# Performance work log

Hardware: AMD Instinct MI355X
Metric: run time of the kernel (lower is better)

The kernel has to match this reference:

```python
import jax, jax.numpy as jnp
import numpy as np

NUM_USERS = 100000
NUM_ITEMS = 50000
EMBED_DIM = 64
N_LAYERS = 3
NNZ = 4800000
BATCH = 16384
N_NODES = NUM_USERS + NUM_ITEMS


def setup_inputs() -> dict:
    key = jax.random.key(0)
    k1, k2, k3, k4, k5, k6, k7 = jax.random.split(key, 7)
    users = jax.random.randint(k1, (BATCH,), 0, NUM_USERS, dtype=jnp.int64 if jax.config.jax_enable_x64 else jnp.int32)
    items = jax.random.randint(k2, (BATCH,), 0, NUM_ITEMS, dtype=jnp.int64 if jax.config.jax_enable_x64 else jnp.int32)
    adj_rows = jax.random.randint(k3, (NNZ,), 0, N_NODES, dtype=jnp.int32)
    adj_cols = jax.random.randint(k4, (NNZ,), 0, N_NODES, dtype=jnp.int32)
    adj_vals = jax.random.uniform(k5, (NNZ,), dtype=jnp.float32)
    user_emb = jax.random.normal(k6, (NUM_USERS, EMBED_DIM), dtype=jnp.float32)
    item_emb = jax.random.normal(k7, (NUM_ITEMS, EMBED_DIM), dtype=jnp.float32)
    return {"users": users, "items": items, "adj_rows": adj_rows,
            "adj_cols": adj_cols, "adj_vals": adj_vals,
            "user_emb": user_emb, "item_emb": item_emb}


def _spmm(rows, cols, vals, x):
    # y = A @ x for COO sparse A: gather source rows, scale, scatter-add to dest
    return jax.ops.segment_sum(vals[:, None] * x[cols], rows, num_segments=N_NODES)


def reference(users, items, adj_rows, adj_cols, adj_vals, user_emb, item_emb):
    ego = jnp.concatenate([user_emb, item_emb], axis=0)  # [N_NODES, D]
    acc = ego
    cur = ego
    for _ in range(N_LAYERS):
        cur = _spmm(adj_rows, adj_cols, adj_vals, cur)
        acc = acc + cur
    mean_emb = acc / jnp.float32(N_LAYERS + 1)
    user_final = mean_emb[:NUM_USERS]
    item_final = mean_emb[NUM_USERS:]
    u = user_final[users]  # [B, D]
    i = item_final[items]  # [B, D]
    return jnp.sum(u * i, axis=-1)  # [B]
```

## Files before the change

### kernel.cpp

```cpp
#include <hip/hip_runtime.h>
#include <hip/hip_bf16.h>

#define NUM_USERS 100000
#define NUM_ITEMS 50000
#define EMBED_DIM 64
#define N_NODES   150000
#define ROW_SHIFT 9
#define ROWS_PER_BUCKET 512
#define B_BUCKETS ((N_NODES + ROWS_PER_BUCKET - 1) / ROWS_PER_BUCKET)
#define NBP 512
#define BIN_CHUNK 2048
#define COL_MASK 0x3FFFF

typedef unsigned short ushort_t;
typedef unsigned int uint_t;

__device__ __forceinline__ float bf16_to_f32(ushort_t u) {
    return __uint_as_float(((unsigned)u) << 16);
}
__device__ __forceinline__ ushort_t f32_to_bf16(float f) {
    return __builtin_bit_cast(ushort_t, __float2bfloat16(f));
}

__global__ void __launch_bounds__(512) k_bin2(const float* __restrict__ ue,
                                              const float* __restrict__ ie,
                                              ushort_t* __restrict__ xb,
                                              const int* __restrict__ rows,
                                              const int* __restrict__ cols,
                                              const float* __restrict__ vals,
                                              int* __restrict__ cursor,
                                              int2* __restrict__ staging,
                                              int nnz, int cap, int g_conv) {
    int t = threadIdx.x;
    if ((int)blockIdx.x < g_conv) {
        int i = blockIdx.x * 512 + t;
        const int n4 = (N_NODES * EMBED_DIM) / 4;
        if (i >= n4) return;
        const int usplit = (NUM_USERS * EMBED_DIM) / 4;
        float4 f = (i < usplit) ? ((const float4*)ue)[i] : ((const float4*)ie)[i - usplit];
        ushort4 o;
        o.x = f32_to_bf16(f.x);
        o.y = f32_to_bf16(f.y);
        o.z = f32_to_bf16(f.z);
        o.w = f32_to_bf16(f.w);
        ((ushort4*)xb)[i] = o;
        return;
    }

    __shared__ int  ccnt[NBP];
    __shared__ int  cpos[NBP];
    __shared__ int  gdst[NBP];
    __shared__ int2 entries[BIN_CHUNK];
    __shared__ ushort_t ebuck[BIN_CHUNK];

    int base = (blockIdx.x - g_conv) * BIN_CHUNK;
    ccnt[t] = 0;
    __syncthreads();

    int myrow[BIN_CHUNK / 512];
#pragma unroll
    for (int k = 0; k < BIN_CHUNK / 512; k++) {
        int idx = base + k * 512 + t;
        int r = (idx < nnz) ? rows[idx] : -1;
        myrow[k] = r;
        if (r >= 0) atomicAdd(&ccnt[r >> ROW_SHIFT], 1);
    }
    __syncthreads();

    int c = ccnt[t];
    cpos[t] = c;
    __syncthreads();
    for (int d = 1; d < NBP; d <<= 1) {
        int y = (t >= d) ? cpos[t - d] : 0;
        __syncthreads();
        cpos[t] += y;
        __syncthreads();
    }
    int total = cpos[NBP - 1];
    int excl = cpos[t] - c;
    __syncthreads();
    cpos[t] = excl;
    __syncthreads();

#pragma unroll
    for (int k = 0; k < BIN_CHUNK / 512; k++) {
        int r = myrow[k];
        if (r >= 0) {
            int idx = base + k * 512 + t;
            int b = r >> ROW_SHIFT;
            int lrow = r & (ROWS_PER_BUCKET - 1);
            int slot = atomicAdd(&cpos[b], 1);
            entries[slot] = make_int2(cols[idx] | (lrow << 18), __float_as_int(vals[idx]));
            ebuck[slot] = (ushort_t)b;
        }
    }
    __syncthreads();

    if (t < B_BUCKETS && ccnt[t] > 0) {
        int g = atomicAdd(&cursor[t], ccnt[t]);
        gdst[t] = t * cap + g - (cpos[t] - ccnt[t]);
    }
    __syncthreads();

    for (int i = t; i < total; i += 512) {
        int eb = ebuck[i];
        int pos = gdst[eb] + i;
        if (pos < (eb + 1) * cap)
            staging[pos] = entries[i];
    }
}

__global__ void __launch_bounds__(512) k_scatter2b(const int2* __restrict__ staging,
                                                   const int* __restrict__ cursor,
                                                   int2* __restrict__ ranges,
                                                   int2* __restrict__ cv, int cap) {
    __shared__ int rc[ROWS_PER_BUCKET];
    int b = blockIdx.x;
    int t = threadIdx.x;
    int rbase = b * cap;
    int cnt_b = cursor[b];
    if (cnt_b > cap) cnt_b = cap;
    int row0 = b << ROW_SHIFT;

    rc[t] = 0;
    __syncthreads();
    for (int i = t; i < cnt_b; i += 512)
        atomicAdd(&rc[staging[rbase + i].x >> 18], 1);
    __syncthreads();

    int c = rc[t];
    for (int d = 1; d < ROWS_PER_BUCKET; d <<= 1) {
        int y = (t >= d) ? rc[t - d] : 0;
        __syncthreads();
        rc[t] += y;
        __syncthreads();
    }
    int excl = rc[t] - c;
    int row = row0 + t;
    if (row < N_NODES) ranges[row] = make_int2(rbase + excl, rbase + excl + c);
    __syncthreads();
    rc[t] = excl;
    __syncthreads();

    for (int i = t; i < cnt_b; i += 512) {
        int2 e = staging[rbase + i];
        int pos = rbase + atomicAdd(&rc[e.x >> 18], 1);
        cv[pos] = make_int2(e.x & COL_MASK, e.y);
    }
}

#define ISSUE8(R, J0)                                                         \
    _Pragma("unroll")                                                         \
    for (int j = 0; j < 8; j++) {                                             \
        int sc = __builtin_amdgcn_readlane(vc, (J0) + j);                     \
        R[j] = xb[((size_t)(uint_t)sc << 6) + lane];                          \
    }

#define CONS8(R, J0)                                                          \
    _Pragma("unroll")                                                         \
    for (int j = 0; j < 8; j++) {                                             \
        float sv = __uint_as_float((uint_t)__builtin_amdgcn_readlane(vv, (J0) + j)); \
        acc += sv * __uint_as_float((uint_t)R[j] << 16);                      \
    }

__device__ __forceinline__ float spmm_row_rl(int beg, int end, int lane,
                                             const int2* __restrict__ cv,
                                             const ushort_t* __restrict__ xb) {
    float acc = 0.f;
#pragma unroll 1
    for (int b = beg; b < end; b += 64) {
        int2 ed = cv[b + lane];
        bool lv = (b + lane) < end;
        int vc = lv ? ed.x : 0;
        int vv = lv ? ed.y : 0;
        int rem = end - b;
        if (rem > 64) rem = 64;

        ushort_t q0[8], q1[8], q2[8], q3[8];
        ISSUE8(q0, 0)
        if (rem > 8)  { ISSUE8(q1, 8)  }
        if (rem > 16) { ISSUE8(q2, 16) }
        if (rem > 24) { ISSUE8(q3, 24) }
        CONS8(q0, 0)
        if (rem > 8)  { CONS8(q1, 8)  }
        if (rem > 16) { CONS8(q2, 16) }
        if (rem > 24) { CONS8(q3, 24) }
        if (rem > 32) {
            ISSUE8(q0, 32)
            if (rem > 40) { ISSUE8(q1, 40) }
            if (rem > 48) { ISSUE8(q2, 48) }
            if (rem > 56) { ISSUE8(q3, 56) }
            CONS8(q0, 32)
            if (rem > 40) { CONS8(q1, 40) }
            if (rem > 48) { CONS8(q2, 48) }
            if (rem > 56) { CONS8(q3, 56) }
        }
    }
    return acc;
}

__global__ void k_spmm(const int2* __restrict__ ranges, const int2* __restrict__ cv,
                       const ushort_t* __restrict__ xb, ushort_t* __restrict__ out) {
    int row = (blockIdx.x * blockDim.x + threadIdx.x) >> 6;
    int lane = threadIdx.x & 63;
    if (row >= N_NODES) return;
    row = __builtin_amdgcn_readfirstlane(row);
    int2 rng = ranges[row];
    int beg = __builtin_amdgcn_readfirstlane(rng.x);
    int end = __builtin_amdgcn_readfirstlane(rng.y);
    float a = spmm_row_rl(beg, end, lane, cv, xb);
    out[(size_t)row * 64 + lane] = f32_to_bf16(a);
}

__global__ void k_last(const int2* __restrict__ ranges, const int2* __restrict__ cv,
                       const int* __restrict__ users, const int* __restrict__ items,
                       const float* __restrict__ ue, const float* __restrict__ ie,
                       const ushort_t* __restrict__ xbA, const ushort_t* __restrict__ xbB,
                       float* __restrict__ out, int batch) {
    int w = (blockIdx.x * blockDim.x + threadIdx.x) >> 6;
    int lane = threadIdx.x & 63;
    if (w >= batch) return;

    int uu = __builtin_amdgcn_readfirstlane(users[w]);
    int ii = __builtin_amdgcn_readfirstlane(items[w]);
    int row_u = uu;
    int row_i = NUM_USERS + ii;

    int2 ru = ranges[row_u];
    float a_u = spmm_row_rl(__builtin_amdgcn_readfirstlane(ru.x),
                            __builtin_amdgcn_readfirstlane(ru.y), lane, cv, xbB);
    int2 ri = ranges[row_i];
    float a_i = spmm_row_rl(__builtin_amdgcn_readfirstlane(ri.x),
                            __builtin_amdgcn_readfirstlane(ri.y), lane, cv, xbB);

    float e_u = ue[(size_t)uu * EMBED_DIM + lane];
    float e_i = ie[(size_t)ii * EMBED_DIM + lane];
    float Au = bf16_to_f32(xbA[(size_t)row_u * 64 + lane]);
    float Bu = bf16_to_f32(xbB[(size_t)row_u * 64 + lane]);
    float Ai = bf16_to_f32(xbA[(size_t)row_i * 64 + lane]);
    float Bi = bf16_to_f32(xbB[(size_t)row_i * 64 + lane]);

    float ux = e_u + Au + Bu + a_u;
    float ix = e_i + Ai + Bi + a_i;

    float p = ux * ix;
#pragma unroll
    for (int d = 32; d > 0; d >>= 1) p += __shfl_down(p, d, 64);
    if (lane == 0) out[w] = p * (1.0f / 16.0f);
}


extern "C" void kernel_launch(void* const* d_in, const int* in_sizes, int n_in,
                              void* d_out, int out_size, void* d_ws, size_t ws_size,
                              hipStream_t stream) {
    const int*   users    = (const int*)  d_in[0];
    const int*   items    = (const int*)  d_in[1];
    const int*   adj_rows = (const int*)  d_in[2];
    const int*   adj_cols = (const int*)  d_in[3];
    const float* adj_vals = (const float*)d_in[4];
    const float* user_emb = (const float*)d_in[5];
    const float* item_emb = (const float*)d_in[6];
    float* out = (float*)d_out;

    const int batch = in_sizes[0];
    const int nnz   = in_sizes[2];

    int cap = ((nnz / B_BUCKETS) * 9 + 7) / 8;
    cap = (cap + 63) & ~63;
    const size_t padded = (size_t)B_BUCKETS * cap;

    char* p = (char*)d_ws;
    auto alloc = [&](size_t bytes) -> char* {
        char* r = p;
        p += (bytes + 255) & ~(size_t)255;
        return r;
    };
    const size_t xb_bytes = (size_t)N_NODES * EMBED_DIM * 2;
    int2*     ranges = (int2*) alloc((size_t)N_NODES * 8);
    int*      cursor = (int*)  alloc(NBP * 4);
    int2*     cv     = (int2*) alloc(padded * 8);
    size_t    region_bytes = padded * 8;
    if (region_bytes < 2 * xb_bytes) region_bytes = 2 * xb_bytes;
    char*     region  = alloc(region_bytes);
    int2*     staging = (int2*)region;
    ushort_t* xbA     = (ushort_t*)region;
    ushort_t* xbB     = (ushort_t*)(region + xb_bytes);
    ushort_t* xb_ego  = (ushort_t*)alloc(xb_bytes);

    const int g_conv  = ((N_NODES * EMBED_DIM / 4) + 511) / 512;
    const int g_bin   = (nnz + BIN_CHUNK - 1) / BIN_CHUNK;
    const int g_nodes = (N_NODES + 3) / 4;
    const int g_batch = (batch + 3) / 4;

    hipMemsetAsync(cursor, 0, NBP * 4, stream);
    k_bin2<<<g_conv + g_bin, 512, 0, stream>>>(user_emb, item_emb, xb_ego,
                                               adj_rows, adj_cols, adj_vals,
                                               cursor, staging, nnz, cap, g_conv);
    k_scatter2b<<<B_BUCKETS, 512, 0, stream>>>(staging, cursor, ranges, cv, cap);

    k_spmm<<<g_nodes, 256, 0, stream>>>(ranges, cv, xb_ego, xbA);

    k_spmm<<<g_nodes, 256, 0, stream>>>(ranges, cv, xbA, xbB);

    k_last<<<g_batch, 256, 0, stream>>>(ranges, cv, users, items,
                                        user_emb, item_emb, xbA, xbB, out, batch);
}
```

Baseline: 430.1 us.

## Replace bucket binning with per-row count, scan, and atomic placement for CSR build

Replaces the two-stage bucket sort (LDS binning into padded staging, then a per-bucket counting sort) with three passes: global per-row atomic counting, a per-bucket scan that writes row ranges and cursors, and a placement pass that reserves each edge's slot with a global atomic and writes column and value directly. This drops the staging buffer and its extra read and write traffic. In exchange it uses millions of global atomics on 150k counters, twice, and adds a kernel launch plus a larger memset. Edge order within a row becomes nondeterministic, so float summation order can vary between runs.

```diff
diff --git a/kernel.cpp b/kernel.cpp
--- a/kernel.cpp
+++ b/kernel.cpp
@@ -8,9 +8,6 @@
 #define ROW_SHIFT 9
 #define ROWS_PER_BUCKET 512
 #define B_BUCKETS ((N_NODES + ROWS_PER_BUCKET - 1) / ROWS_PER_BUCKET)
-#define NBP 512
-#define BIN_CHUNK 2048
-#define COL_MASK 0x3FFFF
 
 typedef unsigned short ushort_t;
 typedef unsigned int uint_t;
@@ -22,15 +19,12 @@
     return __builtin_bit_cast(ushort_t, __float2bfloat16(f));
 }
 
-__global__ void __launch_bounds__(512) k_bin2(const float* __restrict__ ue,
-                                              const float* __restrict__ ie,
-                                              ushort_t* __restrict__ xb,
-                                              const int* __restrict__ rows,
-                                              const int* __restrict__ cols,
-                                              const float* __restrict__ vals,
-                                              int* __restrict__ cursor,
-                                              int2* __restrict__ staging,
-                                              int nnz, int cap, int g_conv) {
+__global__ void __launch_bounds__(512) k_cc(const float* __restrict__ ue,
+                                            const float* __restrict__ ie,
+                                            ushort_t* __restrict__ xb,
+                                            const int* __restrict__ rows,
+                                            int* __restrict__ rc,
+                                            int nnz, int g_conv) {
     int t = threadIdx.x;
     if ((int)blockIdx.x < g_conv) {
         int i = blockIdx.x * 512 + t;
@@ -46,106 +40,68 @@
         ((ushort4*)xb)[i] = o;
         return;
     }
-
-    __shared__ int  ccnt[NBP];
-    __shared__ int  cpos[NBP];
-    __shared__ int  gdst[NBP];
-    __shared__ int2 entries[BIN_CHUNK];
-    __shared__ ushort_t ebuck[BIN_CHUNK];
-
-    int base = (blockIdx.x - g_conv) * BIN_CHUNK;
-    ccnt[t] = 0;
-    __syncthreads();
-
-    int myrow[BIN_CHUNK / 512];
-#pragma unroll
-    for (int k = 0; k < BIN_CHUNK / 512; k++) {
-        int idx = base + k * 512 + t;
-        int r = (idx < nnz) ? rows[idx] : -1;
-        myrow[k] = r;
-        if (r >= 0) atomicAdd(&ccnt[r >> ROW_SHIFT], 1);
-    }
-    __syncthreads();
-
-    int c = ccnt[t];
-    cpos[t] = c;
-    __syncthreads();
-    for (int d = 1; d < NBP; d <<= 1) {
-        int y = (t >= d) ? cpos[t - d] : 0;
-        __syncthreads();
-        cpos[t] += y;
-        __syncthreads();
-    }
-    int total = cpos[NBP - 1];
-    int excl = cpos[t] - c;
-    __syncthreads();
-    cpos[t] = excl;
-    __syncthreads();
-
-#pragma unroll
-    for (int k = 0; k < BIN_CHUNK / 512; k++) {
-        int r = myrow[k];
-        if (r >= 0) {
-            int idx = base + k * 512 + t;
-            int b = r >> ROW_SHIFT;
-            int lrow = r & (ROWS_PER_BUCKET - 1);
-            int slot = atomicAdd(&cpos[b], 1);
-            entries[slot] = make_int2(cols[idx] | (lrow << 18), __float_as_int(vals[idx]));
-            ebuck[slot] = (ushort_t)b;
-        }
-    }
-    __syncthreads();
-
-    if (t < B_BUCKETS && ccnt[t] > 0) {
-        int g = atomicAdd(&cursor[t], ccnt[t]);
-        gdst[t] = t * cap + g - (cpos[t] - ccnt[t]);
-    }
-    __syncthreads();
-
-    for (int i = t; i < total; i += 512) {
-        int eb = ebuck[i];
-        int pos = gdst[eb] + i;
-        if (pos < (eb + 1) * cap)
-            staging[pos] = entries[i];
-    }
-}
-
-__global__ void __launch_bounds__(512) k_scatter2b(const int2* __restrict__ staging,
-                                                   const int* __restrict__ cursor,
-                                                   int2* __restrict__ ranges,
-                                                   int2* __restrict__ cv, int cap) {
-    __shared__ int rc[ROWS_PER_BUCKET];
+    int idx = ((int)(blockIdx.x - g_conv) * 512 + t) * 4;
+    if (idx + 3 < nnz) {
+        int4 r4 = *(const int4*)(rows + idx);
+        atomicAdd(&rc[r4.x], 1);
+        atomicAdd(&rc[r4.y], 1);
+        atomicAdd(&rc[r4.z], 1);
+        atomicAdd(&rc[r4.w], 1);
+    } else {
+        for (int k = idx; k < nnz; k++) atomicAdd(&rc[rows[k]], 1);
+    }
+}
+
+__global__ void __launch_bounds__(512) k_scanb(const int* __restrict__ rc,
+                                               int2* __restrict__ ranges,
+                                               int* __restrict__ cur, int cap) {
+    __shared__ int sc[ROWS_PER_BUCKET];
     int b = blockIdx.x;
     int t = threadIdx.x;
-    int rbase = b * cap;
-    int cnt_b = cursor[b];
-    if (cnt_b > cap) cnt_b = cap;
-    int row0 = b << ROW_SHIFT;
-
-    rc[t] = 0;
+    int row = (b << ROW_SHIFT) + t;
+    int c = (row < N_NODES) ? rc[row] : 0;
+    sc[t] = c;
     __syncthreads();
-    for (int i = t; i < cnt_b; i += 512)
-        atomicAdd(&rc[staging[rbase + i].x >> 18], 1);
-    __syncthreads();
-
-    int c = rc[t];
     for (int d = 1; d < ROWS_PER_BUCKET; d <<= 1) {
-        int y = (t >= d) ? rc[t - d] : 0;
+        int y = (t >= d) ? sc[t - d] : 0;
         __syncthreads();
-        rc[t] += y;
+        sc[t] += y;
         __syncthreads();
     }
-    int excl = rc[t] - c;
-    int row = row0 + t;
-    if (row < N_NODES) ranges[row] = make_int2(rbase + excl, rbase + excl + c);
-    __syncthreads();
-    rc[t] = excl;
-    __syncthreads();
-
-    for (int i = t; i < cnt_b; i += 512) {
-        int2 e = staging[rbase + i];
-        int pos = rbase + atomicAdd(&rc[e.x >> 18], 1);
-        cv[pos] = make_int2(e.x & COL_MASK, e.y);
+    int excl = sc[t] - c;
+    int beg = b * cap + excl;
+    if (row < N_NODES) {
+        ranges[row] = make_int2(beg, beg + c);
+        cur[row] = beg;
+    }
+}
+
+__global__ void __launch_bounds__(512) k_place(const int* __restrict__ rows,
+                                               const int* __restrict__ cols,
+                                               const float* __restrict__ vals,
+                                               int* __restrict__ cur,
+                                               int2* __restrict__ cv,
+                                               int nnz, int cap) {
+    int idx = ((int)blockIdx.x * 512 + (int)threadIdx.x) * 4;
+    if (idx + 3 < nnz) {
+        int4   r4 = *(const int4*)(rows + idx);
+        int4   c4 = *(const int4*)(cols + idx);
+        float4 v4 = *(const float4*)(vals + idx);
+        int p0 = atomicAdd(&cur[r4.x], 1);
+        int p1 = atomicAdd(&cur[r4.y], 1);
+        int p2 = atomicAdd(&cur[r4.z], 1);
+        int p3 = atomicAdd(&cur[r4.w], 1);
+        if (p0 < ((r4.x >> ROW_SHIFT) + 1) * cap) cv[p0] = make_int2(c4.x, __float_as_int(v4.x));
+        if (p1 < ((r4.y >> ROW_SHIFT) + 1) * cap) cv[p1] = make_int2(c4.y, __float_as_int(v4.y));
+        if (p2 < ((r4.z >> ROW_SHIFT) + 1) * cap) cv[p2] = make_int2(c4.z, __float_as_int(v4.z));
+        if (p3 < ((r4.w >> ROW_SHIFT) + 1) * cap) cv[p3] = make_int2(c4.w, __float_as_int(v4.w));
+    } else {
+        for (int k = idx; k < nnz; k++) {
+            int r = rows[k];
+            int pos = atomicAdd(&cur[r], 1);
+            if (pos < ((r >> ROW_SHIFT) + 1) * cap)
+                cv[pos] = make_int2(cols[k], __float_as_int(vals[k]));
+        }
     }
 }
 
@@ -277,26 +233,24 @@
     };
     const size_t xb_bytes = (size_t)N_NODES * EMBED_DIM * 2;
     int2*     ranges = (int2*) alloc((size_t)N_NODES * 8);
-    int*      cursor = (int*)  alloc(NBP * 4);
+    int*      rc     = (int*)  alloc((size_t)N_NODES * 4);
+    int*      cur    = (int*)  alloc((size_t)N_NODES * 4);
     int2*     cv     = (int2*) alloc(padded * 8);
-    size_t    region_bytes = padded * 8;
-    if (region_bytes < 2 * xb_bytes) region_bytes = 2 * xb_bytes;
-    char*     region  = alloc(region_bytes);
-    int2*     staging = (int2*)region;
-    ushort_t* xbA     = (ushort_t*)region;
-    ushort_t* xbB     = (ushort_t*)(region + xb_bytes);
-    ushort_t* xb_ego  = (ushort_t*)alloc(xb_bytes);
+    ushort_t* xbA    = (ushort_t*)alloc(xb_bytes);
+    ushort_t* xbB    = (ushort_t*)alloc(xb_bytes);
+    ushort_t* xb_ego = (ushort_t*)alloc(xb_bytes);
 
     const int g_conv  = ((N_NODES * EMBED_DIM / 4) + 511) / 512;
-    const int g_bin   = (nnz + BIN_CHUNK - 1) / BIN_CHUNK;
+    const int g_edge4 = (nnz + 2047) / 2048;
     const int g_nodes = (N_NODES + 3) / 4;
     const int g_batch = (batch + 3) / 4;
 
-    hipMemsetAsync(cursor, 0, NBP * 4, stream);
-    k_bin2<<<g_conv + g_bin, 512, 0, stream>>>(user_emb, item_emb, xb_ego,
-                                               adj_rows, adj_cols, adj_vals,
-                                               cursor, staging, nnz, cap, g_conv);
-    k_scatter2b<<<B_BUCKETS, 512, 0, stream>>>(staging, cursor, ranges, cv, cap);
+    hipMemsetAsync(rc, 0, (size_t)N_NODES * 4, stream);
+    k_cc<<<g_conv + g_edge4, 512, 0, stream>>>(user_emb, item_emb, xb_ego,
+                                               adj_rows, rc, nnz, g_conv);
+    k_scanb<<<B_BUCKETS, 512, 0, stream>>>(rc, ranges, cur, cap);
+    k_place<<<g_edge4, 512, 0, stream>>>(adj_rows, adj_cols, adj_vals,
+                                         cur, cv, nnz, cap);
 
     k_spmm<<<g_nodes, 256, 0, stream>>>(ranges, cv, xb_ego, xbA);
 
```

After: 769.7 us. 78.9% more time.

## Split per-bucket scatter into global row histogram, scan, and chunked placement

Applied to the files above, without the earlier changes.

Per-row counts are now taken during binning with global atomics, so a separate scan kernel can build row ranges and per-row cursors. Placement then runs across many blocks per bucket (chunked) using global atomics on the cursors. Before, one block per bucket had to do both the counting and the placement passes. This removes the second staging read and raises parallelism for placement. In exchange it adds global atomics in the binning and placement kernels, one more launch, and a larger memset.

```diff
diff --git a/kernel.cpp b/kernel.cpp
--- a/kernel.cpp
+++ b/kernel.cpp
@@ -10,6 +10,7 @@
 #define B_BUCKETS ((N_NODES + ROWS_PER_BUCKET - 1) / ROWS_PER_BUCKET)
 #define NBP 512
 #define BIN_CHUNK 2048
+#define PLACE_CHUNK 2048
 #define COL_MASK 0x3FFFF
 
 typedef unsigned short ushort_t;
@@ -29,6 +30,7 @@
                                               const int* __restrict__ cols,
                                               const float* __restrict__ vals,
                                               int* __restrict__ cursor,
+                                              int* __restrict__ rc,
                                               int2* __restrict__ staging,
                                               int nnz, int cap, int g_conv) {
     int t = threadIdx.x;
@@ -63,7 +65,10 @@
         int idx = base + k * 512 + t;
         int r = (idx < nnz) ? rows[idx] : -1;
         myrow[k] = r;
-        if (r >= 0) atomicAdd(&ccnt[r >> ROW_SHIFT], 1);
+        if (r >= 0) {
+            atomicAdd(&ccnt[r >> ROW_SHIFT], 1);
+            atomicAdd(&rc[r], 1);
+        }
     }
     __syncthreads();
 
@@ -110,41 +115,49 @@
     }
 }
 
-__global__ void __launch_bounds__(512) k_scatter2b(const int2* __restrict__ staging,
-                                                   const int* __restrict__ cursor,
-                                                   int2* __restrict__ ranges,
-                                                   int2* __restrict__ cv, int cap) {
-    __shared__ int rc[ROWS_PER_BUCKET];
+__global__ void __launch_bounds__(512) k_scanb(const int* __restrict__ rc,
+                                               int2* __restrict__ ranges,
+                                               int* __restrict__ cur, int cap) {
+    __shared__ int sc[ROWS_PER_BUCKET];
     int b = blockIdx.x;
     int t = threadIdx.x;
-    int rbase = b * cap;
+    int row = (b << ROW_SHIFT) + t;
+    int c = (row < N_NODES) ? rc[row] : 0;
+    sc[t] = c;
+    __syncthreads();
+    for (int d = 1; d < ROWS_PER_BUCKET; d <<= 1) {
+        int y = (t >= d) ? sc[t - d] : 0;
+        __syncthreads();
+        sc[t] += y;
+        __syncthreads();
+    }
+    int excl = sc[t] - c;
+    int beg = b * cap + excl;
+    if (row < N_NODES) {
+        ranges[row] = make_int2(beg, beg + c);
+        cur[row] = beg;
+    }
+}
+
+__global__ void __launch_bounds__(512) k_rplace(const int2* __restrict__ staging,
+                                                const int* __restrict__ cursor,
+                                                int* __restrict__ cur,
+                                                int2* __restrict__ cv,
+                                                int cap, int chunks) {
+    int b = blockIdx.x / chunks;
+    int k = blockIdx.x - b * chunks;
     int cnt_b = cursor[b];
     if (cnt_b > cap) cnt_b = cap;
+    int lo = k * PLACE_CHUNK;
+    int hi = lo + PLACE_CHUNK;
+    if (hi > cnt_b) hi = cnt_b;
     int row0 = b << ROW_SHIFT;
-
-    rc[t] = 0;
-    __syncthreads();
-    for (int i = t; i < cnt_b; i += 512)
-        atomicAdd(&rc[staging[rbase + i].x >> 18], 1);
-    __syncthreads();
-
-    int c = rc[t];
-    for (int d = 1; d < ROWS_PER_BUCKET; d <<= 1) {
-        int y = (t >= d) ? rc[t - d] : 0;
-        __syncthreads();
-        rc[t] += y;
-        __syncthreads();
-    }
-    int excl = rc[t] - c;
-    int row = row0 + t;
-    if (row < N_NODES) ranges[row] = make_int2(rbase + excl, rbase + excl + c);
-    __syncthreads();
-    rc[t] = excl;
-    __syncthreads();
-
-    for (int i = t; i < cnt_b; i += 512) {
+    int rbase = b * cap;
+#pragma unroll 1
+    for (int i = lo + (int)threadIdx.x; i < hi; i += 512) {
         int2 e = staging[rbase + i];
-        int pos = rbase + atomicAdd(&rc[e.x >> 18], 1);
+        int lrow = e.x >> 18;
+        int pos = atomicAdd(&cur[row0 + lrow], 1);
         cv[pos] = make_int2(e.x & COL_MASK, e.y);
     }
 }
@@ -277,7 +290,9 @@
     };
     const size_t xb_bytes = (size_t)N_NODES * EMBED_DIM * 2;
     int2*     ranges = (int2*) alloc((size_t)N_NODES * 8);
-    int*      cursor = (int*)  alloc(NBP * 4);
+    int*      cursor = (int*)  alloc((NBP + 2 * (size_t)N_NODES) * 4);
+    int*      rc     = cursor + NBP;
+    int*      cur    = rc + N_NODES;
     int2*     cv     = (int2*) alloc(padded * 8);
     size_t    region_bytes = padded * 8;
     if (region_bytes < 2 * xb_bytes) region_bytes = 2 * xb_bytes;
@@ -289,14 +304,17 @@
 
     const int g_conv  = ((N_NODES * EMBED_DIM / 4) + 511) / 512;
     const int g_bin   = (nnz + BIN_CHUNK - 1) / BIN_CHUNK;
+    const int chunks  = (cap + PLACE_CHUNK - 1) / PLACE_CHUNK;
     const int g_nodes = (N_NODES + 3) / 4;
     const int g_batch = (batch + 3) / 4;
 
-    hipMemsetAsync(cursor, 0, NBP * 4, stream);
+    hipMemsetAsync(cursor, 0, (NBP + (size_t)N_NODES) * 4, stream);
     k_bin2<<<g_conv + g_bin, 512, 0, stream>>>(user_emb, item_emb, xb_ego,
                                                adj_rows, adj_cols, adj_vals,
-                                               cursor, staging, nnz, cap, g_conv);
-    k_scatter2b<<<B_BUCKETS, 512, 0, stream>>>(staging, cursor, ranges, cv, cap);
+                                               cursor, rc, staging, nnz, cap, g_conv);
+    k_scanb<<<B_BUCKETS, 512, 0, stream>>>(rc, ranges, cur, cap);
+    k_rplace<<<B_BUCKETS * chunks, 512, 0, stream>>>(staging, cursor, cur, cv,
+                                                     cap, chunks);
 
     k_spmm<<<g_nodes, 256, 0, stream>>>(ranges, cv, xb_ego, xbA);
 
```

After: 692.8 us. 1.61x slower.
